# Kernel optimization log

Measured on AMD Instinct MI355X. Metric: run time of the kernel, lower is better.

Reference implementation:

```python
import jax, jax.numpy as jnp
import numpy as np

B, H, W, C = 8, 64, 64, 512
D = C // 8  # key/query/value projection dim per SAGAN block


def setup_inputs() -> dict:
    key = jax.random.key(0)
    ks = jax.random.split(key, 5)
    scale = 1.0 / np.sqrt(C)
    return {
        "x": jax.random.normal(ks[0], (B, H, W, C), dtype=jnp.float32),
        "Wf": jax.random.normal(ks[1], (C, D), dtype=jnp.float32) * scale,
        "bf": jnp.zeros((D,), dtype=jnp.float32),
        "Wg": jax.random.normal(ks[2], (C, D), dtype=jnp.float32) * scale,
        "bg": jnp.zeros((D,), dtype=jnp.float32),
        "Wh": jax.random.normal(ks[3], (C, D), dtype=jnp.float32) * scale,
        "bh": jnp.zeros((D,), dtype=jnp.float32),
        "Wv": jax.random.normal(ks[4], (D, C), dtype=jnp.float32) * (1.0 / np.sqrt(D)),
        "bv": jnp.zeros((C,), dtype=jnp.float32),
        "gamma": jnp.float32(0.01),
    }


def reference(x, Wf, bf, Wg, bg, Wh, bh, Wv, bv, gamma):
    b, h, w, c = x.shape
    n = h * w
    xf = x.reshape(b, n, c)  # flatten spatial dims: [B, N, C]
    # 1x1 convs == per-position dense projections
    f = xf @ Wf + bf  # [B, N, D]
    g = xf @ Wg + bg  # [B, N, D]
    hh = xf @ Wh + bh  # [B, N, D]
    # unscaled attention logits, softmax over keys (axis=-1)
    s = jnp.einsum("bnd,bmd->bnm", f, g)  # [B, N, N]
    attn = jax.nn.softmax(s, axis=-1)
    context = jnp.einsum("bnm,bmd->bnd", attn, hh)  # [B, N, D]
    # v conv (1x1) applied to gamma-scaled context, residual add
    o = (gamma * context) @ Wv + bv + xf  # [B, N, C]
    return o.reshape(b, h, w, c)
```

## Files before the change

### kernel.cpp

```cpp
#include <hip/hip_runtime.h>
#include <hip/hip_bf16.h>
#include <math.h>


typedef short v8s __attribute__((ext_vector_type(8)));
typedef unsigned short v4u __attribute__((ext_vector_type(4)));
typedef float v4f __attribute__((ext_vector_type(4)));

#define BB 8
#define NN 4096
#define CC 512
#define DD 64

__device__ __forceinline__ unsigned short f2bf(float f){
  union { float f; unsigned u; } v; v.f = f;
  unsigned r = (v.u + 0x7FFF + ((v.u >> 16) & 1)) >> 16;
  return (unsigned short)r;
}

__global__ void transpose_w(const float* __restrict__ Wf,
                            const float* __restrict__ Wg,
                            const float* __restrict__ Wh,
                            const float* __restrict__ Wv,
                            unsigned short* __restrict__ Wt,
                            unsigned short* __restrict__ Wvt){
  int idx = blockIdx.x * 256 + threadIdx.x;
  if (idx < 3 * DD * CC){
    int p = idx / (DD * CC); int rem = idx % (DD * CC);
    int d = rem / CC; int c = rem % CC;
    const float* W = (p == 0) ? Wf : ((p == 1) ? Wg : Wh);
    Wt[idx] = f2bf(W[c * DD + d]);
  } else {
    int idx2 = idx - 3 * DD * CC;
    if (idx2 < CC * DD){
      int c = idx2 / DD; int d = idx2 % DD;
      Wvt[idx2] = f2bf(Wv[d * CC + c]);
    }
  }
}

__global__ __launch_bounds__(256) void proj_kernel(
    const float* __restrict__ x,
    const unsigned short* __restrict__ Wt,
    const float* __restrict__ bf_,
    const float* __restrict__ bg_,
    const float* __restrict__ bh_,
    unsigned short* __restrict__ f,
    unsigned short* __restrict__ g,
    unsigned short* __restrict__ ht)
{
  __shared__ __align__(16) short lA[64][72];
  __shared__ __align__(16) short lB[192][72];
  int t = threadIdx.x;
  int w = t >> 6, lane = t & 63;
  int quad = lane >> 4, l16 = lane & 15;
  int rowbase = blockIdx.x * 64;
  int m0 = w * 16;

  v4f acc[12];
  #pragma unroll
  for (int i = 0; i < 12; i++) acc[i] = (v4f){0.f, 0.f, 0.f, 0.f};

  for (int kt = 0; kt < 8; ++kt){
    int k0 = kt * 64;
    #pragma unroll
    for (int r = 0; r < 4; r++){
      int chunk = t + r * 256;
      int row = chunk >> 4, c4 = chunk & 15;
      v4f xv = *(const v4f*)(x + (rowbase + row) * 512 + k0 + c4 * 4);
      v4u bv4 = { f2bf(xv[0]), f2bf(xv[1]), f2bf(xv[2]), f2bf(xv[3]) };
      *(v4u*)&lA[row][c4 * 4] = bv4;
    }
    #pragma unroll
    for (int r = 0; r < 6; r++){
      int chunk = t + r * 256;
      int row = chunk >> 3, c8 = chunk & 7;
      *(v8s*)&lB[row][c8 * 8] = *(const v8s*)(Wt + row * 512 + k0 + c8 * 8);
    }
    __syncthreads();
    v8s A0 = *(const v8s*)&lA[m0 + l16][quad * 8];
    v8s A1 = *(const v8s*)&lA[m0 + l16][quad * 8 + 32];
    #pragma unroll
    for (int cb = 0; cb < 12; ++cb){
      v8s b0 = *(const v8s*)&lB[cb * 16 + l16][quad * 8];
      v8s b1 = *(const v8s*)&lB[cb * 16 + l16][quad * 8 + 32];
      acc[cb] = __builtin_amdgcn_mfma_f32_16x16x32_bf16(A0, b0, acc[cb], 0, 0, 0);
      acc[cb] = __builtin_amdgcn_mfma_f32_16x16x32_bf16(A1, b1, acc[cb], 0, 0, 0);
    }
    __syncthreads();
  }
  #pragma unroll
  for (int cb = 0; cb < 12; ++cb){
    int col = cb * 16 + l16;
    int p = col >> 6, d = col & 63;
    const float* bias = (p == 0) ? bf_ : ((p == 1) ? bg_ : bh_);
    float bb = bias[d];
    #pragma unroll
    for (int r = 0; r < 4; r++){
      int gr = rowbase + m0 + quad * 4 + r;
      float val = acc[cb][r] + bb;
      if (p == 0)      f[gr * 64 + d] = f2bf(val * 1.44269504f);
      else if (p == 1) g[gr * 64 + d] = f2bf(val);
      else {
        int b = gr >> 12, n = gr & 4095;
        ht[(b * 64 + d) * 4096 + n] = f2bf(val);
      }
    }
  }
}

__global__ __launch_bounds__(256) void flash_kernel(
    const unsigned short* __restrict__ f,
    const unsigned short* __restrict__ g,
    const unsigned short* __restrict__ ht,
    float* __restrict__ Opart,
    float* __restrict__ lipart,
    unsigned short* __restrict__ ctx,
    int niter, int direct)
{
  __shared__ __align__(16) short lK[64][72];
  __shared__ __align__(16) short lV[64][72];
  __shared__ __align__(16) short lP[4][16][72];
  int t = threadIdx.x;
  int w = t >> 6, lane = t & 63;
  int quad = lane >> 4, l16 = lane & 15;
  int qt = blockIdx.x;
  int sp = blockIdx.y;
  int b  = blockIdx.z;
  int q0 = qt * 64;
  int m0 = w * 16;

  const unsigned short* fb = f  + b * NN * 64;
  const unsigned short* gb = g  + b * NN * 64;
  const unsigned short* hb = ht + b * 64 * NN;

  v8s QB0 = *(const v8s*)(fb + (q0 + m0 + l16) * 64 + quad * 8);
  v8s QB1 = *(const v8s*)(fb + (q0 + m0 + l16) * 64 + quad * 8 + 32);

  float rsum = 0.f;
  v4f O[4];
  #pragma unroll
  for (int cb = 0; cb < 4; cb++) O[cb] = (v4f){0.f, 0.f, 0.f, 0.f};

  int j0 = sp * niter;
  for (int jj = 0; jj < niter; ++jj){
    int j = j0 + jj;
    #pragma unroll
    for (int r = 0; r < 2; r++){
      int chunk = t + r * 256;
      int row = chunk >> 3, c8 = chunk & 7;
      *(v8s*)&lK[row][c8 * 8] = *(const v8s*)(gb + (j * 64 + row) * 64 + c8 * 8);
      *(v8s*)&lV[row][c8 * 8] = *(const v8s*)(hb + row * 4096 + j * 64 + c8 * 8);
    }
    __syncthreads();

    v4f st[4];
    #pragma unroll
    for (int cb = 0; cb < 4; cb++){
      v8s a0 = *(const v8s*)&lK[cb * 16 + l16][quad * 8];
      v8s a1 = *(const v8s*)&lK[cb * 16 + l16][quad * 8 + 32];
      v4f z = (v4f){0.f, 0.f, 0.f, 0.f};
      z = __builtin_amdgcn_mfma_f32_16x16x32_bf16(a0, QB0, z, 0, 0, 0);
      st[cb] = __builtin_amdgcn_mfma_f32_16x16x32_bf16(a1, QB1, z, 0, 0, 0);
    }

    #pragma unroll
    for (int cb = 0; cb < 4; cb++){
      float p0 = exp2f(st[cb][0]);
      float p1 = exp2f(st[cb][1]);
      float p2 = exp2f(st[cb][2]);
      float p3 = exp2f(st[cb][3]);
      rsum += (p0 + p1) + (p2 + p3);
      unsigned d0 = __builtin_amdgcn_perm(__float_as_uint(p1), __float_as_uint(p0), 0x07060302u);
      unsigned d1 = __builtin_amdgcn_perm(__float_as_uint(p3), __float_as_uint(p2), 0x07060302u);
      uint2 pk; pk.x = d0; pk.y = d1;
      *(uint2*)&lP[w][l16][cb * 16 + quad * 4] = pk;
    }

    v8s PA0 = *(const v8s*)&lP[w][l16][quad * 8];
    v8s PA1 = *(const v8s*)&lP[w][l16][quad * 8 + 32];
    #pragma unroll
    for (int cb = 0; cb < 4; cb++){
      v8s vb0 = *(const v8s*)&lV[cb * 16 + l16][quad * 8];
      v8s vb1 = *(const v8s*)&lV[cb * 16 + l16][quad * 8 + 32];
      O[cb] = __builtin_amdgcn_mfma_f32_16x16x32_bf16(PA0, vb0, O[cb], 0, 0, 0);
      O[cb] = __builtin_amdgcn_mfma_f32_16x16x32_bf16(PA1, vb1, O[cb], 0, 0, 0);
    }
    __syncthreads();
  }

  rsum += __shfl_xor(rsum, 16, 64);
  rsum += __shfl_xor(rsum, 32, 64);

  if (direct){
    float inv[4];
    #pragma unroll
    for (int r = 0; r < 4; r++)
      inv[r] = 1.0f / __shfl(rsum, quad * 4 + r, 64);
    #pragma unroll
    for (int cb = 0; cb < 4; cb++)
      #pragma unroll
      for (int r = 0; r < 4; r++){
        int row = q0 + m0 + quad * 4 + r;
        ctx[(b * NN + row) * 64 + cb * 16 + l16] = f2bf(O[cb][r] * inv[r]);
      }
  } else {
    int bf = (b * 64 + qt) * 4 + sp;
    if (quad == 0) lipart[bf * 64 + m0 + l16] = rsum;
    float* Ob = Opart + bf * 4096;
    #pragma unroll
    for (int cb = 0; cb < 4; cb++)
      #pragma unroll
      for (int r = 0; r < 4; r++)
        Ob[(m0 + quad * 4 + r) * 64 + cb * 16 + l16] = O[cb][r];
  }
}

__global__ __launch_bounds__(256) void reduce_kernel(
    const float* __restrict__ Opart,
    const float* __restrict__ lipart,
    unsigned short* __restrict__ ctx)
{
  int idx = blockIdx.x * 256 + threadIdx.x;
  int bqt = idx >> 12;
  int rem = idx & 4095;
  int rl  = rem >> 6;
  const float* Ob  = Opart  + (size_t)bqt * 4 * 4096;
  const float* lib = lipart + bqt * 4 * 64;
  float s  = (Ob[rem] + Ob[4096 + rem]) + (Ob[8192 + rem] + Ob[12288 + rem]);
  float li = (lib[rl] + lib[64 + rl]) + (lib[128 + rl] + lib[192 + rl]);
  ctx[idx] = f2bf(s / li);
}

__global__ __launch_bounds__(256) void outproj_kernel(
    const unsigned short* __restrict__ ctx,
    const unsigned short* __restrict__ Wvt,
    const float* __restrict__ bv,
    const float* __restrict__ x,
    const float* __restrict__ gamma_p,
    float* __restrict__ out)
{
  __shared__ __align__(16) short lA[64][72];
  __shared__ __align__(16) short lB[128][72];
  int t = threadIdx.x;
  int w = t >> 6, lane = t & 63;
  int quad = lane >> 4, l16 = lane & 15;
  int rowbase = blockIdx.x * 64;
  int colbase = blockIdx.y * 128;
  float gamma = *gamma_p;

  #pragma unroll
  for (int r = 0; r < 2; r++){
    int chunk = t + r * 256;
    int row = chunk >> 3, c8 = chunk & 7;
    *(v8s*)&lA[row][c8 * 8] = *(const v8s*)(ctx + (rowbase + row) * 64 + c8 * 8);
  }
  #pragma unroll
  for (int r = 0; r < 4; r++){
    int chunk = t + r * 256;
    int row = chunk >> 3, c8 = chunk & 7;
    *(v8s*)&lB[row][c8 * 8] = *(const v8s*)(Wvt + (colbase + row) * 64 + c8 * 8);
  }
  __syncthreads();
  int m0 = w * 16;
  v8s A0 = *(const v8s*)&lA[m0 + l16][quad * 8];
  v8s A1 = *(const v8s*)&lA[m0 + l16][quad * 8 + 32];
  v4f acc[8];
  #pragma unroll
  for (int cb = 0; cb < 8; cb++){
    v8s b0 = *(const v8s*)&lB[cb * 16 + l16][quad * 8];
    v8s b1 = *(const v8s*)&lB[cb * 16 + l16][quad * 8 + 32];
    v4f z = (v4f){0.f, 0.f, 0.f, 0.f};
    z = __builtin_amdgcn_mfma_f32_16x16x32_bf16(A0, b0, z, 0, 0, 0);
    acc[cb] = __builtin_amdgcn_mfma_f32_16x16x32_bf16(A1, b1, z, 0, 0, 0);
  }
  #pragma unroll
  for (int cb = 0; cb < 8; cb++){
    int col = colbase + cb * 16 + l16;
    float bvv = bv[col];
    #pragma unroll
    for (int r = 0; r < 4; r++){
      int gr = rowbase + m0 + quad * 4 + r;
      out[gr * 512 + col] = gamma * acc[cb][r] + bvv + x[gr * 512 + col];
    }
  }
}

extern "C" void kernel_launch(void* const* d_in, const int* in_sizes, int n_in,
                              void* d_out, int out_size, void* d_ws, size_t ws_size,
                              hipStream_t stream) {
  const float* x   = (const float*)d_in[0];
  const float* Wf  = (const float*)d_in[1];
  const float* bf_ = (const float*)d_in[2];
  const float* Wg  = (const float*)d_in[3];
  const float* bg  = (const float*)d_in[4];
  const float* Wh  = (const float*)d_in[5];
  const float* bh  = (const float*)d_in[6];
  const float* Wv  = (const float*)d_in[7];
  const float* bv  = (const float*)d_in[8];
  const float* gam = (const float*)d_in[9];
  float* out = (float*)d_out;

  char* ws = (char*)d_ws;
  unsigned short* Wt  = (unsigned short*)(ws);
  unsigned short* Wvt = (unsigned short*)(ws + 196608);
  unsigned short* f   = (unsigned short*)(ws + 262144);
  unsigned short* g   = (unsigned short*)(ws + 4456448);
  unsigned short* ht  = (unsigned short*)(ws + 8650752);
  unsigned short* ctx = (unsigned short*)(ws + 12845056);
  float* Opart  = (float*)(ws + 17039360);
  float* lipart = (float*)(ws + 50593792);

  transpose_w<<<512, 256, 0, stream>>>(Wf, Wg, Wh, Wv, Wt, Wvt);
  proj_kernel<<<512, 256, 0, stream>>>(x, Wt, bf_, bg, bh, f, g, ht);

  bool split = (ws_size >= (size_t)51118080);
  if (split){
    flash_kernel<<<dim3(64, 4, 8), 256, 0, stream>>>(f, g, ht, Opart, lipart, ctx, 16, 0);
    reduce_kernel<<<8192, 256, 0, stream>>>(Opart, lipart, ctx);
  } else {
    flash_kernel<<<dim3(64, 1, 8), 256, 0, stream>>>(f, g, ht, nullptr, nullptr, ctx, 64, 1);
  }
  outproj_kernel<<<dim3(512, 4), 256, 0, stream>>>(ctx, Wvt, bv, x, gam, out);
}
```

Before: 236.6 us.

## Use direct global-to-LDS loads with swizzle, vectorize projection and reduce stores

The flash kernel now stages K and V tiles with global_load_lds 16-byte transfers into an XOR-swizzled, unpadded LDS layout, so the data no longer passes through VGPRs. The projection kernel converts x with packed bf16 conversion and wider per-thread loads. It also transposes the h output through LDS so it can be written as coalesced 16-byte stores instead of scattered 2-byte writes. The reduce kernel processes four elements per thread with vector loads and packed stores. Together these cut memory-instruction count and uncoalesced traffic, at the cost of relying on swizzle index correctness and async-load ordering.

```diff
diff --git a/kernel.cpp b/kernel.cpp
--- a/kernel.cpp
+++ b/kernel.cpp
@@ -5,6 +5,7 @@
 
 typedef short v8s __attribute__((ext_vector_type(8)));
 typedef unsigned short v4u __attribute__((ext_vector_type(4)));
+typedef unsigned v4i __attribute__((ext_vector_type(4)));
 typedef float v4f __attribute__((ext_vector_type(4)));
 
 #define BB 8
@@ -16,6 +17,24 @@
   union { float f; unsigned u; } v; v.f = f;
   unsigned r = (v.u + 0x7FFF + ((v.u >> 16) & 1)) >> 16;
   return (unsigned short)r;
+}
+
+#if __has_builtin(__builtin_amdgcn_cvt_pk_bf16_f32)
+typedef __bf16 bf2_t __attribute__((ext_vector_type(2)));
+__device__ __forceinline__ unsigned pkbf(float a, float b){
+  bf2_t r = __builtin_amdgcn_cvt_pk_bf16_f32(a, b);
+  union { bf2_t v; unsigned u; } c; c.v = r; return c.u;
+}
+#else
+__device__ __forceinline__ unsigned pkbf(float a, float b){
+  return (unsigned)f2bf(a) | ((unsigned)f2bf(b) << 16);
+}
+#endif
+
+__device__ __forceinline__ void gload_lds16(const void* g, void* l){
+  __builtin_amdgcn_global_load_lds(
+      (const __attribute__((address_space(1))) void*)g,
+      (__attribute__((address_space(3))) void*)l, 16, 0, 0);
 }
 
 __global__ void transpose_w(const float* __restrict__ Wf,
@@ -61,15 +80,21 @@
   #pragma unroll
   for (int i = 0; i < 12; i++) acc[i] = (v4f){0.f, 0.f, 0.f, 0.f};
 
+  int arow = t >> 2, aq4 = t & 3;
   for (int kt = 0; kt < 8; ++kt){
     int k0 = kt * 64;
-    #pragma unroll
-    for (int r = 0; r < 4; r++){
-      int chunk = t + r * 256;
-      int row = chunk >> 4, c4 = chunk & 15;
-      v4f xv = *(const v4f*)(x + (rowbase + row) * 512 + k0 + c4 * 4);
-      v4u bv4 = { f2bf(xv[0]), f2bf(xv[1]), f2bf(xv[2]), f2bf(xv[3]) };
-      *(v4u*)&lA[row][c4 * 4] = bv4;
+    {
+      const float* xp = x + (rowbase + arow) * 512 + k0 + aq4 * 16;
+      v4f a0 = *(const v4f*)(xp);
+      v4f a1 = *(const v4f*)(xp + 4);
+      v4f a2 = *(const v4f*)(xp + 8);
+      v4f a3 = *(const v4f*)(xp + 12);
+      v4i c0 = { pkbf(a0[0],a0[1]), pkbf(a0[2],a0[3]),
+                 pkbf(a1[0],a1[1]), pkbf(a1[2],a1[3]) };
+      v4i c1 = { pkbf(a2[0],a2[1]), pkbf(a2[2],a2[3]),
+                 pkbf(a3[0],a3[1]), pkbf(a3[2],a3[3]) };
+      *(v4i*)&lA[arow][aq4 * 16]     = c0;
+      *(v4i*)&lA[arow][aq4 * 16 + 8] = c1;
     }
     #pragma unroll
     for (int r = 0; r < 6; r++){
@@ -89,23 +114,44 @@
     }
     __syncthreads();
   }
-  #pragma unroll
-  for (int cb = 0; cb < 12; ++cb){
+
+  #pragma unroll
+  for (int cb = 0; cb < 8; ++cb){
     int col = cb * 16 + l16;
     int p = col >> 6, d = col & 63;
-    const float* bias = (p == 0) ? bf_ : ((p == 1) ? bg_ : bh_);
-    float bb = bias[d];
+    float bb = (p == 0) ? bf_[d] : bg_[d];
     #pragma unroll
     for (int r = 0; r < 4; r++){
       int gr = rowbase + m0 + quad * 4 + r;
       float val = acc[cb][r] + bb;
-      if (p == 0)      f[gr * 64 + d] = f2bf(val * 1.44269504f);
-      else if (p == 1) g[gr * 64 + d] = f2bf(val);
-      else {
-        int b = gr >> 12, n = gr & 4095;
-        ht[(b * 64 + d) * 4096 + n] = f2bf(val);
-      }
-    }
+      if (p == 0) f[gr * 64 + d] = f2bf(val * 1.44269504f);
+      else        g[gr * 64 + d] = f2bf(val);
+    }
+  }
+
+  short (*lT)[65] = (short(*)[65])lB;
+  #pragma unroll
+  for (int cb = 8; cb < 12; ++cb){
+    int d = (cb - 8) * 16 + l16;
+    float bb = bh_[d];
+    #pragma unroll
+    for (int r = 0; r < 4; r++)
+      lT[m0 + quad * 4 + r][d] = (short)f2bf(acc[cb][r] + bb);
+  }
+  __syncthreads();
+  {
+    int dd = t >> 2, nb = t & 3;
+    v8s h0, h1;
+    #pragma unroll
+    for (int i = 0; i < 8; i++){
+      h0[i] = lT[nb * 16 + i][dd];
+      h1[i] = lT[nb * 16 + 8 + i][dd];
+    }
+    int bidx = rowbase >> 12;
+    int n0 = (rowbase & 4095) + nb * 16;
+    unsigned short* hp = ht + ((size_t)(bidx * 64 + dd)) * 4096 + n0;
+    *(v8s*)hp = h0;
+    *(v8s*)(hp + 8) = h1;
   }
 }
 
@@ -118,15 +164,13 @@
     unsigned short* __restrict__ ctx,
     int niter, int direct)
 {
-  __shared__ __align__(16) short lK[64][72];
-  __shared__ __align__(16) short lV[64][72];
+  __shared__ __align__(16) short lK[64 * 64];
+  __shared__ __align__(16) short lV[64 * 64];
   __shared__ __align__(16) short lP[4][16][72];
   int t = threadIdx.x;
   int w = t >> 6, lane = t & 63;
   int quad = lane >> 4, l16 = lane & 15;
-  int qt = blockIdx.x;
-  int sp = blockIdx.y;
-  int b  = blockIdx.z;
+  int qt = blockIdx.x, sp = blockIdx.y, b = blockIdx.z;
   int q0 = qt * 64;
   int m0 = w * 16;
 
@@ -137,28 +181,44 @@
   v8s QB0 = *(const v8s*)(fb + (q0 + m0 + l16) * 64 + quad * 8);
   v8s QB1 = *(const v8s*)(fb + (q0 + m0 + l16) * 64 + quad * 8 + 32);
 
+  int j0 = sp * niter;
+  const char* srcK[2]; const char* srcV[2];
+  char* dstK[2]; char* dstV[2];
+  #pragma unroll
+  for (int k = 0; k < 2; k++){
+    int row = w * 16 + k * 8 + (lane >> 3);
+    int c = (lane & 7) ^ (row & 7);
+    srcK[k] = (const char*)gb + (size_t)j0 * 8192 + row * 128 + c * 16;
+    srcV[k] = (const char*)hb + (size_t)row * 8192 + (size_t)j0 * 128 + c * 16;
+    dstK[k] = (char*)lK + w * 2048 + k * 1024;
+    dstV[k] = (char*)lV + w * 2048 + k * 1024;
+  }
+
+  int ph = quad ^ (l16 & 7);
+  const short* kA0 = lK + l16 * 64 + ph * 8;
+  const short* kA1 = lK + l16 * 64 + (ph ^ 4) * 8;
+  const short* vB0 = lV + l16 * 64 + ph * 8;
+  const short* vB1 = lV + l16 * 64 + (ph ^ 4) * 8;
+
   float rsum = 0.f;
   v4f O[4];
   #pragma unroll
   for (int cb = 0; cb < 4; cb++) O[cb] = (v4f){0.f, 0.f, 0.f, 0.f};
 
-  int j0 = sp * niter;
   for (int jj = 0; jj < niter; ++jj){
-    int j = j0 + jj;
-    #pragma unroll
-    for (int r = 0; r < 2; r++){
-      int chunk = t + r * 256;
-      int row = chunk >> 3, c8 = chunk & 7;
-      *(v8s*)&lK[row][c8 * 8] = *(const v8s*)(gb + (j * 64 + row) * 64 + c8 * 8);
-      *(v8s*)&lV[row][c8 * 8] = *(const v8s*)(hb + row * 4096 + j * 64 + c8 * 8);
+    #pragma unroll
+    for (int k = 0; k < 2; k++){
+      gload_lds16(srcK[k], dstK[k]);
+      gload_lds16(srcV[k], dstV[k]);
+      srcK[k] += 8192; srcV[k] += 128;
     }
     __syncthreads();
 
     v4f st[4];
     #pragma unroll
     for (int cb = 0; cb < 4; cb++){
-      v8s a0 = *(const v8s*)&lK[cb * 16 + l16][quad * 8];
-      v8s a1 = *(const v8s*)&lK[cb * 16 + l16][quad * 8 + 32];
+      v8s a0 = *(const v8s*)(kA0 + cb * 1024);
+      v8s a1 = *(const v8s*)(kA1 + cb * 1024);
       v4f z = (v4f){0.f, 0.f, 0.f, 0.f};
       z = __builtin_amdgcn_mfma_f32_16x16x32_bf16(a0, QB0, z, 0, 0, 0);
       st[cb] = __builtin_amdgcn_mfma_f32_16x16x32_bf16(a1, QB1, z, 0, 0, 0);
@@ -181,8 +241,8 @@
     v8s PA1 = *(const v8s*)&lP[w][l16][quad * 8 + 32];
     #pragma unroll
     for (int cb = 0; cb < 4; cb++){
-      v8s vb0 = *(const v8s*)&lV[cb * 16 + l16][quad * 8];
-      v8s vb1 = *(const v8s*)&lV[cb * 16 + l16][quad * 8 + 32];
+      v8s vb0 = *(const v8s*)(vB0 + cb * 1024);
+      v8s vb1 = *(const v8s*)(vB1 + cb * 1024);
       O[cb] = __builtin_amdgcn_mfma_f32_16x16x32_bf16(PA0, vb0, O[cb], 0, 0, 0);
       O[cb] = __builtin_amdgcn_mfma_f32_16x16x32_bf16(PA1, vb1, O[cb], 0, 0, 0);
     }
@@ -207,7 +267,7 @@
   } else {
     int bf = (b * 64 + qt) * 4 + sp;
     if (quad == 0) lipart[bf * 64 + m0 + l16] = rsum;
-    float* Ob = Opart + bf * 4096;
+    float* Ob = Opart + (size_t)bf * 4096;
     #pragma unroll
     for (int cb = 0; cb < 4; cb++)
       #pragma unroll
@@ -221,15 +281,20 @@
     const float* __restrict__ lipart,
     unsigned short* __restrict__ ctx)
 {
-  int idx = blockIdx.x * 256 + threadIdx.x;
-  int bqt = idx >> 12;
-  int rem = idx & 4095;
+  int i4 = blockIdx.x * 256 + threadIdx.x;
+  int bqt = i4 >> 10;
+  int rem = (i4 & 1023) << 2;
   int rl  = rem >> 6;
   const float* Ob  = Opart  + (size_t)bqt * 4 * 4096;
   const float* lib = lipart + bqt * 4 * 64;
-  float s  = (Ob[rem] + Ob[4096 + rem]) + (Ob[8192 + rem] + Ob[12288 + rem]);
+  v4f s = *(const v4f*)(Ob + rem);
+  s = s + *(const v4f*)(Ob + 4096  + rem);
+  s = s + *(const v4f*)(Ob + 8192  + rem);
+  s = s + *(const v4f*)(Ob + 12288 + rem);
   float li = (lib[rl] + lib[64 + rl]) + (lib[128 + rl] + lib[192 + rl]);
-  ctx[idx] = f2bf(s / li);
+  float inv = 1.0f / li;
+  uint2 o; o.x = pkbf(s[0] * inv, s[1] * inv); o.y = pkbf(s[2] * inv, s[3] * inv);
+  *(uint2*)(ctx + (size_t)bqt * 4096 + rem) = o;
 }
 
 __global__ __launch_bounds__(256) void outproj_kernel(
@@ -317,7 +382,7 @@
   bool split = (ws_size >= (size_t)51118080);
   if (split){
     flash_kernel<<<dim3(64, 4, 8), 256, 0, stream>>>(f, g, ht, Opart, lipart, ctx, 16, 0);
-    reduce_kernel<<<8192, 256, 0, stream>>>(Opart, lipart, ctx);
+    reduce_kernel<<<2048, 256, 0, stream>>>(Opart, lipart, ctx);
   } else {
     flash_kernel<<<dim3(64, 1, 8), 256, 0, stream>>>(f, g, ht, nullptr, nullptr, ctx, 64, 1);
   }
```

New measurement: 228.9 us. 3.2% less time.
